# Kernel tuning notes

Hardware: AMD Instinct MI355X
Metric: run time of the kernel (lower is better)

The kernel has to match this reference:

```python
import jax, jax.numpy as jnp
import numpy as np

B, N, E, K, D, V = 16, 2048, 4096, 32, 768, 1024
T = N + E  # tokens per graph (nodes then edges)


def setup_inputs() -> dict:
    key = jax.random.key(0)
    ks = jax.random.split(key, 7)
    node_data = jax.random.randint(ks[0], (B * N, D), 0, V, dtype=jnp.int32)
    edge_data = jax.random.randint(ks[1], (B * E, D), 0, V, dtype=jnp.int32)
    edge_index = jax.random.randint(ks[2], (2, B * E), 0, N, dtype=jnp.int32)  # per-graph local ids
    lap_eigvec = jax.random.normal(ks[3], (B * N, K), jnp.float32)  # precomputed lap eigvecs, already padded/truncated to K
    emb_table = jax.random.normal(ks[4], (V, 1), jnp.float32) * 0.02
    lap_w = jax.random.normal(ks[5], (D, 2 * K), jnp.float32) * (0.02 / np.sqrt(12.0))
    order_emb = jax.random.normal(ks[6], (2, D), jnp.float32) * 0.02
    node_num = jnp.full((B,), N, jnp.int32)
    edge_num = jnp.full((B,), E, jnp.int32)
    ar = jnp.arange(N, dtype=jnp.int32)
    node_pi = jnp.broadcast_to(jnp.stack([ar, ar], -1)[None], (B, N, 2))  # node tokens: (i, i)
    edge_pi = edge_index.reshape(2, B, E).transpose(1, 2, 0)  # edge tokens: (src, dst)
    padded_index = jnp.concatenate([node_pi, edge_pi], axis=1)  # [B, T, 2]
    padded_node_mask = jnp.concatenate([jnp.ones((B, N), bool), jnp.zeros((B, E), bool)], 1)
    padded_edge_mask = ~padded_node_mask
    padding_mask = jnp.zeros((B, T), bool)
    return dict(edge_index=edge_index, edge_data=edge_data, node_data=node_data,
                node_num=node_num, edge_num=edge_num, padded_index=padded_index,
                padding_mask=padding_mask, padded_node_mask=padded_node_mask,
                padded_edge_mask=padded_edge_mask, lap_eigvec=lap_eigvec,
                emb_table=emb_table, lap_w=lap_w, order_emb=order_emb)


def _mask_scatter(mask_flat, src):
    """Emulate padded[mask] = src: for each padded slot, gather the matching
    compacted row (cumsum(mask)-1 gives the rank of each True position)."""
    pos = jnp.cumsum(mask_flat) - 1
    return jnp.where(mask_flat[:, None], src[pos], jnp.zeros((), src.dtype))


def reference(edge_index, edge_data, node_data, node_num, edge_num, padded_index,
              padding_mask, padded_node_mask, padded_edge_mask,
              lap_eigvec, emb_table, lap_w, order_emb):
    b, t = padding_mask.shape
    d = node_data.shape[-1]
    # embedding with output dim 1, squeezed -> feature dim == token-grid width
    node_feature = emb_table[node_data, 0]  # [sum_node, D]
    edge_feature = emb_table[edge_data, 0]  # [sum_edge, D]
    nm = padded_node_mask.reshape(-1)
    em = padded_edge_mask.reshape(-1)
    padded_feature = (_mask_scatter(nm, node_feature)
                      + _mask_scatter(em, edge_feature)).reshape(b, t, d)
    # --- lap node-id embedding (get_index_embed + lap_encoder) ---
    max_n = lap_eigvec.shape[0] // b  # uniform graphs -> static max_n
    node_mask = (jnp.arange(max_n)[None, :] < node_num[:, None]).reshape(-1)
    padded_node_id = _mask_scatter(node_mask, lap_eigvec).reshape(b, max_n, -1)  # [B, max_n, K]
    index_embed = jax.vmap(lambda p, i: p[i])(padded_node_id, padded_index)  # [B, T, 2, K]
    index_embed = index_embed.reshape(b, t, -1)  # [B, T, 2K]
    padded_feature = padded_feature + index_embed @ lap_w.T
    # --- type (order) embedding ---
    order = (padded_index[..., 0] == padded_index[..., 1]).astype(jnp.int32)
    padded_feature = padded_feature + order_emb[order]
    return jnp.where(padding_mask[..., None], jnp.zeros((), padded_feature.dtype), padded_feature)
```

## Files before the change

### kernel.cpp

```cpp
#include <hip/hip_runtime.h>


constexpr int CB = 16;
constexpr int CN = 2048;
constexpr int CE = 4096;
constexpr int CT = 6144;
constexpr int CK = 32;
constexpr int CD = 768;
constexpr int CV = 1024;
constexpr int TPB = 256;
constexpr int TOK = 128;
constexpr int CPG = CT / TOK;

using f32x4  = __attribute__((ext_vector_type(4))) float;
using i32x4  = __attribute__((ext_vector_type(4))) int;
using bf16x8 = __attribute__((ext_vector_type(8))) short;

__device__ __forceinline__ short f2bf(float f) {
    union { float f; unsigned u; } x{f};
    unsigned r = x.u + 0x7fffu + ((x.u >> 16) & 1u);
    return (short)(r >> 16);
}
__device__ __forceinline__ bf16x8 cvt8(f32x4 a, f32x4 b) {
    bf16x8 r;
    r[0] = f2bf(a[0]); r[1] = f2bf(a[1]); r[2] = f2bf(a[2]); r[3] = f2bf(a[3]);
    r[4] = f2bf(b[0]); r[5] = f2bf(b[1]); r[6] = f2bf(b[2]); r[7] = f2bf(b[3]);
    return r;
}

__global__ __launch_bounds__(TPB, 3) void gft_mfma(
    const int* __restrict__ node_data,
    const int* __restrict__ edge_data,
    const int* __restrict__ padded_index,
    const float* __restrict__ eig,
    const float* __restrict__ emb,
    const float* __restrict__ lap_w,
    const float* __restrict__ order_emb,
    float* __restrict__ out)
{
    __shared__ float s_emb[CV];
    __shared__ int2 s_pi[TOK];
    __shared__ __align__(16) float s_acc[16][260];

    const int tid  = threadIdx.x;
    const int lane = tid & 63;
    const int wid  = tid >> 6;
    const int b = blockIdx.x / CPG, c = blockIdx.x % CPG;
    const int dbase = blockIdx.y * 256;
    const int dloc  = dbase + wid * 64;
    const int dq    = dbase + 4 * lane;

    for (int i = tid; i < CV; i += TPB) s_emb[i] = emb[i];
    {
        const int2* pi = (const int2*)padded_index + (size_t)(b * CT + c * TOK);
        if (tid < TOK) s_pi[tid] = pi[tid];
    }

    const int* __restrict__ dptr = (c * TOK < CN)
        ? node_data + ((size_t)b * CN + c * TOK) * CD
        : edge_data + ((size_t)b * CE + (c * TOK - CN)) * CD;
    const float* __restrict__ eig_b = eig + (size_t)b * CN * CK;
    float* __restrict__ outp = out + ((size_t)(b * CT + c * TOK)) * CD;

    const int koff = (lane >> 4) * 8;
    const int dl   = lane & 15;

    bf16x8 bw[4][2];
#pragma unroll
    for (int n = 0; n < 4; ++n) {
        const float* wr = lap_w + (size_t)(dloc + 16 * n + dl) * (2 * CK) + koff;
        bw[n][0] = cvt8(*(const f32x4*)wr,        *(const f32x4*)(wr + 4));
        bw[n][1] = cvt8(*(const f32x4*)(wr + 32), *(const f32x4*)(wr + 36));
    }
    const f32x4 oe0q = *(const f32x4*)(order_emb + dq);
    const f32x4 oe1q = *(const f32x4*)(order_emb + CD + dq);
    __syncthreads();

    f32x4 q00, q01, q10, q11;
    {
        const int2 ia = s_pi[dl];
        const float* e0 = eig_b + (size_t)ia.x * CK + koff;
        const float* e1 = eig_b + (size_t)ia.y * CK + koff;
        q00 = *(const f32x4*)e0; q01 = *(const f32x4*)(e0 + 4);
        q10 = *(const f32x4*)e1; q11 = *(const f32x4*)(e1 + 4);
    }

    for (int t0 = 0; t0 < TOK; t0 += 16) {
        i32x4 tokv[4];
#pragma unroll
        for (int s = 0; s < 4; ++s)
            tokv[s] = __builtin_nontemporal_load(
                (const i32x4*)(dptr + (size_t)(t0 + 4 * s + wid) * CD + dq));

        const bf16x8 a0 = cvt8(q00, q01);
        const bf16x8 a1 = cvt8(q10, q11);

        if (t0 + 16 < TOK) {
            const int2 ia = s_pi[t0 + 16 + dl];
            const float* e0 = eig_b + (size_t)ia.x * CK + koff;
            const float* e1 = eig_b + (size_t)ia.y * CK + koff;
            q00 = *(const f32x4*)e0; q01 = *(const f32x4*)(e0 + 4);
            q10 = *(const f32x4*)e1; q11 = *(const f32x4*)(e1 + 4);
        }

        f32x4 acc[4];
#pragma unroll
        for (int n = 0; n < 4; ++n) {
            f32x4 z = {0.f, 0.f, 0.f, 0.f};
            z = __builtin_amdgcn_mfma_f32_16x16x32_bf16(a0, bw[n][0], z, 0, 0, 0);
            acc[n] = __builtin_amdgcn_mfma_f32_16x16x32_bf16(a1, bw[n][1], z, 0, 0, 0);
        }

        asm volatile("s_waitcnt lgkmcnt(0)" ::: "memory");
        __builtin_amdgcn_s_barrier();
#pragma unroll
        for (int n = 0; n < 4; ++n)
#pragma unroll
            for (int r = 0; r < 4; ++r)
                s_acc[(lane >> 4) * 4 + r][wid * 64 + 16 * n + dl] = acc[n][r];
        asm volatile("s_waitcnt lgkmcnt(0)" ::: "memory");
        __builtin_amdgcn_s_barrier();

#pragma unroll
        for (int s = 0; s < 4; ++s) {
            const int tr = 4 * s + wid;
            const int2 i01 = s_pi[t0 + tr];
            const f32x4 av = *(const f32x4*)&s_acc[tr][4 * lane];
            const f32x4 oe = (i01.x == i01.y) ? oe1q : oe0q;
            f32x4 y;
            y[0] = av[0] + s_emb[tokv[s][0]] + oe[0];
            y[1] = av[1] + s_emb[tokv[s][1]] + oe[1];
            y[2] = av[2] + s_emb[tokv[s][2]] + oe[2];
            y[3] = av[3] + s_emb[tokv[s][3]] + oe[3];
            __builtin_nontemporal_store(
                y, (f32x4*)(outp + (size_t)(t0 + tr) * CD + dq));
        }
    }
}

extern "C" void kernel_launch(void* const* d_in, const int* in_sizes, int n_in,
                              void* d_out, int out_size, void* d_ws, size_t ws_size,
                              hipStream_t stream) {
    const int*   edge_data    = (const int*)d_in[1];
    const int*   node_data    = (const int*)d_in[2];
    const int*   padded_index = (const int*)d_in[5];
    const float* lap_eigvec   = (const float*)d_in[9];
    const float* emb_table    = (const float*)d_in[10];
    const float* lap_w        = (const float*)d_in[11];
    const float* order_emb    = (const float*)d_in[12];
    float* out = (float*)d_out;

    dim3 grid(CB * CPG, CD / 256);
    gft_mfma<<<grid, TPB, 0, stream>>>(node_data, edge_data, padded_index,
                                       lap_eigvec, emb_table, lap_w, order_emb, out);
}
```

Before: 135.9 us.

## Double-buffer accumulator tile and prefetch next token-id rows one iteration ahead

Splits the shared accumulator into two buffers so one of the two barriers per iteration can be dropped. It also software-pipelines the token-id global loads so the next 16 rows are fetched during the current iteration's MFMA and epilogue. Embedding lookups are hoisted ahead of the MFMAs. The cost is extra registers (tokn, embv) and double the LDS for s_acc, which may reduce occupancy under launch_bounds(256,3).

New measurement: 132.9 us. -2.2%, faster.

```diff
diff --git a/kernel.cpp b/kernel.cpp
--- a/kernel.cpp
+++ b/kernel.cpp
@@ -40,7 +40,7 @@
 {
     __shared__ float s_emb[CV];
     __shared__ int2 s_pi[TOK];
-    __shared__ __align__(16) float s_acc[16][260];
+    __shared__ __align__(16) float s_acc[2][16][260];
 
     const int tid  = threadIdx.x;
     const int lane = tid & 63;
@@ -84,23 +84,36 @@
         q00 = *(const f32x4*)e0; q01 = *(const f32x4*)(e0 + 4);
         q10 = *(const f32x4*)e1; q11 = *(const f32x4*)(e1 + 4);
     }
+    i32x4 tokc[4];
+#pragma unroll
+    for (int s = 0; s < 4; ++s)
+        tokc[s] = __builtin_nontemporal_load(
+            (const i32x4*)(dptr + (size_t)(4 * s + wid) * CD + dq));
 
-    for (int t0 = 0; t0 < TOK; t0 += 16) {
-        i32x4 tokv[4];
+    for (int it = 0; it < TOK / 16; ++it) {
+        const int t0 = it * 16;
+
+        float embv[4][4];
 #pragma unroll
         for (int s = 0; s < 4; ++s)
-            tokv[s] = __builtin_nontemporal_load(
-                (const i32x4*)(dptr + (size_t)(t0 + 4 * s + wid) * CD + dq));
+#pragma unroll
+            for (int j = 0; j < 4; ++j)
+                embv[s][j] = s_emb[tokc[s][j]];
 
         const bf16x8 a0 = cvt8(q00, q01);
         const bf16x8 a1 = cvt8(q10, q11);
 
-        if (t0 + 16 < TOK) {
+        i32x4 tokn[4];
+        if (it + 1 < TOK / 16) {
             const int2 ia = s_pi[t0 + 16 + dl];
             const float* e0 = eig_b + (size_t)ia.x * CK + koff;
             const float* e1 = eig_b + (size_t)ia.y * CK + koff;
             q00 = *(const f32x4*)e0; q01 = *(const f32x4*)(e0 + 4);
             q10 = *(const f32x4*)e1; q11 = *(const f32x4*)(e1 + 4);
+#pragma unroll
+            for (int s = 0; s < 4; ++s)
+                tokn[s] = __builtin_nontemporal_load(
+                    (const i32x4*)(dptr + (size_t)(t0 + 16 + 4 * s + wid) * CD + dq));
         }
 
         f32x4 acc[4];
@@ -111,13 +124,11 @@
             acc[n] = __builtin_amdgcn_mfma_f32_16x16x32_bf16(a1, bw[n][1], z, 0, 0, 0);
         }
 
-        asm volatile("s_waitcnt lgkmcnt(0)" ::: "memory");
-        __builtin_amdgcn_s_barrier();
 #pragma unroll
         for (int n = 0; n < 4; ++n)
 #pragma unroll
             for (int r = 0; r < 4; ++r)
-                s_acc[(lane >> 4) * 4 + r][wid * 64 + 16 * n + dl] = acc[n][r];
+                s_acc[it & 1][(lane >> 4) * 4 + r][wid * 64 + 16 * n + dl] = acc[n][r];
         asm volatile("s_waitcnt lgkmcnt(0)" ::: "memory");
         __builtin_amdgcn_s_barrier();
 
@@ -125,16 +136,19 @@
         for (int s = 0; s < 4; ++s) {
             const int tr = 4 * s + wid;
             const int2 i01 = s_pi[t0 + tr];
-            const f32x4 av = *(const f32x4*)&s_acc[tr][4 * lane];
+            const f32x4 av = *(const f32x4*)&s_acc[it & 1][tr][4 * lane];
             const f32x4 oe = (i01.x == i01.y) ? oe1q : oe0q;
             f32x4 y;
-            y[0] = av[0] + s_emb[tokv[s][0]] + oe[0];
-            y[1] = av[1] + s_emb[tokv[s][1]] + oe[1];
-            y[2] = av[2] + s_emb[tokv[s][2]] + oe[2];
-            y[3] = av[3] + s_emb[tokv[s][3]] + oe[3];
+            y[0] = av[0] + embv[s][0] + oe[0];
+            y[1] = av[1] + embv[s][1] + oe[1];
+            y[2] = av[2] + embv[s][2] + oe[2];
+            y[3] = av[3] + embv[s][3] + oe[3];
             __builtin_nontemporal_store(
                 y, (f32x4*)(outp + (size_t)(t0 + tr) * CD + dq));
         }
+
+#pragma unroll
+        for (int s = 0; s < 4; ++s) tokc[s] = tokn[s];
     }
 }
 
```
